# Performance work log

Hardware: AMD Instinct MI355X
Metric: run time of the kernel (lower is better)

The kernel has to match this reference:

```python
import jax, jax.numpy as jnp
import numpy as np

N, M, P, C_IN, C_OUT = 100000, 50000, 1600000, 128, 128
NEG_SLOPE = 0.2


def segment_softmax(w, seg, num):
    # numerically-stable softmax of w over segments defined by seg
    m = jax.ops.segment_max(w, seg, num_segments=num)
    e = jnp.exp(w - m[seg])
    s = jax.ops.segment_sum(e, seg, num_segments=num)
    return e / s[seg]


def setup_inputs() -> dict:
    key = jax.random.key(0)
    ks = jax.random.split(key, 8)
    scale = 1.0 / np.sqrt(C_IN)
    return {
        "X": jax.random.normal(ks[0], (N, C_IN), dtype=jnp.float32),
        "pair_v": jax.random.randint(ks[1], (P,), 0, N, dtype=jnp.int32),
        "pair_e": jax.random.randint(ks[2], (P,), 0, M, dtype=jnp.int32),
        "src_v": jax.random.randint(ks[3], (P,), 0, N, dtype=jnp.int32),
        "W_theta": jax.random.normal(ks[4], (C_OUT, C_IN), dtype=jnp.float32) * scale,
        "b_theta": jax.random.normal(ks[5], (C_OUT,), dtype=jnp.float32) * scale,
        "w_src": jax.random.normal(ks[6], (C_OUT,), dtype=jnp.float32) * scale,
        "w_dst": jax.random.normal(ks[7], (C_OUT,), dtype=jnp.float32) * scale,
    }


def reference(X, pair_v, pair_e, src_v, W_theta, b_theta, w_src, w_dst):
    # theta: linear projection (eval mode: dropout = identity, no BN)
    H = X @ W_theta.T + b_theta                      # [N, C_OUT]

    # per-pair attention scores: atten_src(H)[src] + atten_dst(H)[dst]
    s = H @ w_src                                    # [N]
    d = H @ w_dst                                    # [N]
    score = jax.nn.leaky_relu(s[src_v] + d[pair_v], NEG_SLOPE)  # [P]
    score = jnp.clip(score, 0.001, 5.0)

    # degrees
    ones = jnp.ones((P,), dtype=H.dtype)
    de = jnp.maximum(jax.ops.segment_sum(ones, pair_e, num_segments=M), 1.0)  # [M]
    dv = jnp.maximum(jax.ops.segment_sum(ones, pair_v, num_segments=N), 1.0)  # [N]

    dv_isqrt = dv ** -0.5
    Xs = H * dv_isqrt[:, None]
    Xe = jax.ops.segment_sum(Xs[pair_v], pair_e, num_segments=M) / de[:, None]  # [M, C]
    Hs = jax.ops.segment_sum(Xe[pair_e], pair_v, num_segments=N) * dv_isqrt[:, None]

    # v2v(aggr='softmax_then_sum', e2v_weight=score):
    #   v2e softmax_then_sum with unit weights == per-edge mean
    Xe1 = jax.ops.segment_sum(Hs[pair_v], pair_e, num_segments=M) / de[:, None]
    #   e2v: segment-softmax the scores per destination vertex, weighted sum
    alpha = segment_softmax(score, pair_v, N)        # [P]
    Xv1 = jax.ops.segment_sum(alpha[:, None] * Xe1[pair_e], pair_v, num_segments=N)

    # v2v(aggr='mean', v2e_aggr='softmax_then_sum'):
    #   v2e softmax_then_sum with unit weights == per-edge mean; e2v mean
    Xe2 = jax.ops.segment_sum(Xv1[pair_v], pair_e, num_segments=M) / de[:, None]
    Xv2 = jax.ops.segment_sum(Xe2[pair_e], pair_v, num_segments=N) / dv[:, None]

    # is_last=False: ELU activation (dropout identity in eval)
    return jax.nn.elu(Xv2)
```

## Files before the change

### kernel.cpp

```cpp
#include <hip/hip_runtime.h>
#include <math.h>

#define M_EDGES 50000
#define CHUNK 1024

#define NBMAX 200
#define TILE_E 4096
#define TILE_V 4096
#define CAPL_E 44
#define CAPL_V 32

typedef unsigned int u32;
typedef unsigned short u16;

__device__ __forceinline__ float bflo(u32 u) { return __uint_as_float(u << 16); }
__device__ __forceinline__ float bfhi(u32 u) { return __uint_as_float(u & 0xffff0000u); }
__device__ __forceinline__ u32 packbf(float x, float y) {
  u32 a = __float_as_uint(x); a += 0x7fffu + ((a >> 16) & 1u);
  u32 b = __float_as_uint(y); b += 0x7fffu + ((b >> 16) & 1u);
  return (a >> 16) | (b & 0xffff0000u);
}
__device__ __forceinline__ int swz(int k) { return ((k >> 2) & 7) << 2; }

__global__ __launch_bounds__(256) void bin_edge_kernel(
    const int* __restrict__ pair_e, const int* __restrict__ pair_v,
    u32* __restrict__ out, int* __restrict__ gcur,
    int P, int SE, int NB) {
  __shared__ int lcnt[NBMAX];
  __shared__ int gbase[NBMAX];
  __shared__ u32 stage[NBMAX][CAPL_E];
  const int tid = (int)threadIdx.x;
  const int p0 = blockIdx.x * TILE_E;
  const int pend = (p0 + TILE_E < P) ? p0 + TILE_E : P;
  const u32 maskE = (1u << SE) - 1u;
  for (int b = tid; b < NB; b += 256) lcnt[b] = 0;
  __syncthreads();
  for (int p = p0 + tid; p < pend; p += 256) {
    const int e = pair_e[p];
    const int v = pair_v[p];
    const int b = e >> SE;
    const u32 entry = (u32)v | (((u32)e & maskE) << 17);
    const int pos = atomicAdd(&lcnt[b], 1);
    if (pos < CAPL_E) stage[b][pos] = entry;
    else out[atomicAdd(&gcur[b], 1)] = entry;
  }
  __syncthreads();
  for (int b = tid; b < NB; b += 256) {
    const int n = lcnt[b] < CAPL_E ? lcnt[b] : CAPL_E;
    gbase[b] = atomicAdd(&gcur[b], n);
  }
  __syncthreads();
  const int wv = tid >> 6, lane = tid & 63;
  for (int b = wv; b < NB; b += 4) {
    const int n = lcnt[b] < CAPL_E ? lcnt[b] : CAPL_E;
    if (lane < n) out[gbase[b] + lane] = stage[b][lane];
  }
}

__global__ __launch_bounds__(256) void bin_vtx_kernel(
    const int* __restrict__ pair_e, const int* __restrict__ pair_v,
    const int* __restrict__ src_v,
    uint2* __restrict__ out, int* __restrict__ gcur,
    int P, int SV, int NB) {
  __shared__ int lcnt[NBMAX];
  __shared__ int gbase[NBMAX];
  __shared__ uint2 stage[NBMAX][CAPL_V];
  const int tid = (int)threadIdx.x;
  const int p0 = blockIdx.x * TILE_V;
  const int pend = (p0 + TILE_V < P) ? p0 + TILE_V : P;
  const u32 maskV = (1u << SV) - 1u;
  for (int b = tid; b < NB; b += 256) lcnt[b] = 0;
  __syncthreads();
  for (int p = p0 + tid; p < pend; p += 256) {
    const int e = pair_e[p];
    const int v = pair_v[p];
    const int s = src_v[p];
    const int b = v >> SV;
    uint2 entry;
    entry.x = ((u32)v & maskV) | ((u32)e << SV);
    entry.y = (u32)s;
    const int pos = atomicAdd(&lcnt[b], 1);
    if (pos < CAPL_V) stage[b][pos] = entry;
    else out[atomicAdd(&gcur[b], 1)] = entry;
  }
  __syncthreads();
  for (int b = tid; b < NB; b += 256) {
    const int n = lcnt[b] < CAPL_V ? lcnt[b] : CAPL_V;
    gbase[b] = atomicAdd(&gcur[b], n);
  }
  __syncthreads();
  const int wv = tid >> 6, lane = tid & 63;
  for (int b = wv; b < NB; b += 4) {
    const int n = lcnt[b] < CAPL_V ? lcnt[b] : CAPL_V;
    if (lane < n) out[gbase[b] + lane] = stage[b][lane];
  }
}

__global__ void init_gcur_kernel(int* __restrict__ ge, int* __restrict__ gv,
                                 int NBE, int NBV, int capgE, int capgV) {
  const int t = (int)threadIdx.x;
  if (t < NBE) ge[t] = t * capgE;
  if (t < NBV) gv[t] = t * capgV;
}

__global__ __launch_bounds__(256) void bucket_hist_kernel(
    const u32* __restrict__ entE, const int* __restrict__ gcurE, int* __restrict__ cnt_e,
    const uint2* __restrict__ entV, const int* __restrict__ gcurV, int* __restrict__ cnt_v,
    int NBE, int SE, int capgE, int SV, int capgV, int M, int N) {
  __shared__ int h[1024];
  const int b = (int)blockIdx.x;
  const int tid = (int)threadIdx.x;
  if (b < NBE) {
    const int nb = 1 << SE;
    for (int t = tid; t < nb; t += 256) h[t] = 0;
    __syncthreads();
    const int end = gcurE[b];
    for (int i = b * capgE + tid; i < end; i += 256)
      atomicAdd(&h[entE[i] >> 17], 1);
    __syncthreads();
    const int base = b << SE;
    for (int t = tid; t < nb; t += 256)
      if (base + t < M) cnt_e[base + t] = h[t];
  } else {
    const int bb = b - NBE;
    const int nb = 1 << SV;
    for (int t = tid; t < nb; t += 256) h[t] = 0;
    __syncthreads();
    const int end = gcurV[bb];
    const u32 mask = (1u << SV) - 1u;
    for (int i = bb * capgV + tid; i < end; i += 256)
      atomicAdd(&h[entV[i].x & mask], 1);
    __syncthreads();
    const int base = bb << SV;
    for (int t = tid; t < nb; t += 256)
      if (base + t < N) cnt_v[base + t] = h[t];
  }
}

__global__ __launch_bounds__(512) void unbin_edge_kernel(
    const u32* __restrict__ ent, const int* __restrict__ gcur,
    int* __restrict__ cur_e, int* __restrict__ edge_vtx,
    int SE, int capg) {
  const int b = blockIdx.x;
  const int end = gcur[b];
  const int ebase = b << SE;
  for (int i = b * capg + (int)threadIdx.x; i < end; i += 512) {
    const u32 w = ent[i];
    const int v = (int)(w & 0x1ffffu);
    const int e = ebase + (int)(w >> 17);
    edge_vtx[atomicAdd(&cur_e[e], 1)] = v;
  }
}

__global__ __launch_bounds__(512) void unbin_vtx_kernel(
    const uint2* __restrict__ ent, const int* __restrict__ gcur,
    int* __restrict__ cur_v, int2* __restrict__ vtx_es,
    const float* __restrict__ svec, const float* __restrict__ dvec,
    int SV, int capg) {
  const int b = blockIdx.x;
  const int end = gcur[b];
  const int vbase = b << SV;
  const u32 maskV = (1u << SV) - 1u;
  for (int i = b * capg + (int)threadIdx.x; i < end; i += 512) {
    const uint2 w = ent[i];
    const int v = vbase + (int)(w.x & maskV);
    const int e = (int)(w.x >> SV);
    float sc = svec[w.y] + dvec[v];
    sc = sc > 0.f ? sc : 0.2f * sc;
    sc = fminf(fmaxf(sc, 0.001f), 5.0f);
    vtx_es[atomicAdd(&cur_v[v], 1)] = make_int2(e, __float_as_int(__expf(sc)));
  }
}

__global__ __launch_bounds__(1024) void blocksum_kernel(
    const int* __restrict__ cnt_e, const int* __restrict__ cnt_v,
    int* __restrict__ part, int CE, int M, int N) {
  const int b = blockIdx.x;
  const int* cnt;
  int n, chunk;
  if (b < CE) { cnt = cnt_e; n = M; chunk = b; }
  else        { cnt = cnt_v; n = N; chunk = b - CE; }
  const int i = chunk * CHUNK + (int)threadIdx.x;
  int x = (i < n) ? cnt[i] : 0;
#pragma unroll
  for (int m = 32; m >= 1; m >>= 1) x += __shfl_xor(x, m, 64);
  __shared__ int ws[16];
  if ((threadIdx.x & 63) == 0) ws[threadIdx.x >> 6] = x;
  __syncthreads();
  if (threadIdx.x == 0) {
    int t = 0;
#pragma unroll
    for (int q = 0; q < 16; ++q) t += ws[q];
    part[b] = t;
  }
}

__global__ __launch_bounds__(256) void partscan_kernel(
    int* __restrict__ part, int CE, int CV,
    int* __restrict__ off_e, int* __restrict__ off_v, int M, int N) {
  __shared__ int sh[256];
  const int tid = (int)threadIdx.x;
  for (int s = 0; s < 2; ++s) {
    const int base = s ? CE : 0;
    const int count = s ? CV : CE;
    int x = (tid < count) ? part[base + tid] : 0;
    sh[tid] = x;
    __syncthreads();
    for (int ofs = 1; ofs < 256; ofs <<= 1) {
      int v = (tid >= ofs) ? sh[tid - ofs] : 0;
      __syncthreads();
      sh[tid] += v;
      __syncthreads();
    }
    if (tid < count) part[base + tid] = sh[tid] - x;
    if (tid == 0) {
      const int tot = sh[count - 1];
      if (s == 0) off_e[M] = tot; else off_v[N] = tot;
    }
    __syncthreads();
  }
}

__global__ __launch_bounds__(1024) void blockscan_kernel(
    const int* __restrict__ cnt_e, const int* __restrict__ cnt_v,
    const int* __restrict__ part,
    int* __restrict__ off_e, int* __restrict__ off_v,
    int* __restrict__ cur_e, int* __restrict__ cur_v,
    float* __restrict__ de_inv, float* __restrict__ dv_inv, float* __restrict__ dv_isqrt,
    int CE, int M, int N) {
  __shared__ int sh[CHUNK];
  const int b = blockIdx.x;
  const int tid = (int)threadIdx.x;
  const int* cnt;
  int n, chunk;
  int *off, *cur;
  float *i1, *i2;
  if (b < CE) { cnt = cnt_e; n = M; chunk = b;      off = off_e; cur = cur_e; i1 = de_inv; i2 = nullptr; }
  else        { cnt = cnt_v; n = N; chunk = b - CE; off = off_v; cur = cur_v; i1 = dv_inv; i2 = dv_isqrt; }
  const int i = chunk * CHUNK + tid;
  const int x = (i < n) ? cnt[i] : 0;
  sh[tid] = x;
  __syncthreads();
  for (int ofs = 1; ofs < CHUNK; ofs <<= 1) {
    int v = (tid >= ofs) ? sh[tid - ofs] : 0;
    __syncthreads();
    sh[tid] += v;
    __syncthreads();
  }
  if (i < n) {
    const int o = part[b] + sh[tid] - x;
    off[i] = o;
    cur[i] = o;
    const float m = (float)(x > 1 ? x : 1);
    i1[i] = 1.0f / m;
    if (i2) i2[i] = 1.0f / sqrtf(m);
  }
}

__global__ __launch_bounds__(256) void gemm_kernel(
    const float* __restrict__ X, const float* __restrict__ W,
    const float* __restrict__ bias, const float* __restrict__ wsrc,
    const float* __restrict__ wdst, const float* __restrict__ dv_isqrt,
    u16* __restrict__ Hb, float* __restrict__ s_out, float* __restrict__ d_out,
    int N) {
  __shared__ float lw[64 * 128];
  __shared__ float lx[32 * 128];
  const int tid = threadIdx.x;
  const int row0 = blockIdx.x * 32;

  for (int g = tid; g < 32 * 32; g += 256) {
    const int r = g >> 5;
    const int k4 = (g & 31) << 2;
    int rr = row0 + r;
    if (rr >= N) rr = N - 1;
    *(float4*)(lx + r * 128 + k4) = *(const float4*)(X + (size_t)rr * 128 + k4);
  }

  const int tx = tid & 31;
  const int ty = tid >> 5;
  const int c0 = tx << 2;
  const int r0 = ty << 2;
  float acc[4][4] = {};

  for (int half = 0; half < 2; ++half) {
    __syncthreads();
    for (int g = tid; g < 128 * 16; g += 256) {
      const int c = g >> 4;
      const int kk4 = (g & 15) << 2;
      const float4 v = *(const float4*)(W + (size_t)c * 128 + half * 64 + kk4);
      const int s = swz(kk4);
      lw[(kk4 + 0) * 128 + (c ^ s)] = v.x;
      lw[(kk4 + 1) * 128 + (c ^ s)] = v.y;
      lw[(kk4 + 2) * 128 + (c ^ s)] = v.z;
      lw[(kk4 + 3) * 128 + (c ^ s)] = v.w;
    }
    __syncthreads();
#pragma unroll 8
    for (int kk = 0; kk < 64; ++kk) {
      const int k = half * 64 + kk;
      const float4 wv = *(const float4*)(lw + kk * 128 + (c0 ^ swz(kk)));
      const float x0 = lx[(r0 + 0) * 128 + k];
      const float x1 = lx[(r0 + 1) * 128 + k];
      const float x2 = lx[(r0 + 2) * 128 + k];
      const float x3 = lx[(r0 + 3) * 128 + k];
      acc[0][0] += x0 * wv.x; acc[0][1] += x0 * wv.y; acc[0][2] += x0 * wv.z; acc[0][3] += x0 * wv.w;
      acc[1][0] += x1 * wv.x; acc[1][1] += x1 * wv.y; acc[1][2] += x1 * wv.z; acc[1][3] += x1 * wv.w;
      acc[2][0] += x2 * wv.x; acc[2][1] += x2 * wv.y; acc[2][2] += x2 * wv.z; acc[2][3] += x2 * wv.w;
      acc[3][0] += x3 * wv.x; acc[3][1] += x3 * wv.y; acc[3][2] += x3 * wv.z; acc[3][3] += x3 * wv.w;
    }
  }

  const float4 bv = *(const float4*)(bias + c0);
  const float4 sv = *(const float4*)(wsrc + c0);
  const float4 dv = *(const float4*)(wdst + c0);

#pragma unroll
  for (int r = 0; r < 4; ++r) {
    const int row = row0 + r0 + r;
    float4 h;
    h.x = acc[r][0] + bv.x; h.y = acc[r][1] + bv.y;
    h.z = acc[r][2] + bv.z; h.w = acc[r][3] + bv.w;
    float ps = h.x * sv.x + h.y * sv.y + h.z * sv.z + h.w * sv.w;
    float pd = h.x * dv.x + h.y * dv.y + h.z * dv.z + h.w * dv.w;
#pragma unroll
    for (int m = 16; m >= 1; m >>= 1) {
      ps += __shfl_xor(ps, m, 64);
      pd += __shfl_xor(pd, m, 64);
    }
    if (row < N) {
      const float sc = dv_isqrt[row];
      uint2 pk;
      pk.x = packbf(h.x * sc, h.y * sc);
      pk.y = packbf(h.z * sc, h.w * sc);
      *(uint2*)(Hb + (size_t)row * 128 + c0) = pk;
      if (tx == 0) { s_out[row] = ps; d_out[row] = pd; }
    }
  }
}

#define ACC8(r, p)                                         \
  a[0] += bflo((r).x) * (p); a[1] += bfhi((r).x) * (p);    \
  a[2] += bflo((r).y) * (p); a[3] += bfhi((r).y) * (p);    \
  a[4] += bflo((r).z) * (p); a[5] += bfhi((r).z) * (p);    \
  a[6] += bflo((r).w) * (p); a[7] += bfhi((r).w) * (p);

__global__ __launch_bounds__(256) void seg_pass_kernel(
    const u16* __restrict__ src, void* __restrict__ dst,
    const int* __restrict__ off, const int* __restrict__ lst, int ls,
    const float* __restrict__ post_scale,
    int nseg, int final_mode) {
  const int seg = blockIdx.x * 4 + ((int)threadIdx.x >> 6);
  if (seg >= nseg) return;
  const int lane = (int)threadIdx.x & 63;
  const int q = lane >> 4;
  const int cl = lane & 15;
  const int beg = off[seg], end = off[seg + 1];
  float a[8] = {};
  int i = beg;
  for (; i + 16 <= end; i += 16) {
    const int j0 = lst[(size_t)(i + q) * ls];
    const int j1 = lst[(size_t)(i + 4 + q) * ls];
    const int j2 = lst[(size_t)(i + 8 + q) * ls];
    const int j3 = lst[(size_t)(i + 12 + q) * ls];
    const uint4 r0 = *(const uint4*)(src + (size_t)j0 * 128 + cl * 8);
    const uint4 r1 = *(const uint4*)(src + (size_t)j1 * 128 + cl * 8);
    const uint4 r2 = *(const uint4*)(src + (size_t)j2 * 128 + cl * 8);
    const uint4 r3 = *(const uint4*)(src + (size_t)j3 * 128 + cl * 8);
    ACC8(r0, 1.0f) ACC8(r1, 1.0f) ACC8(r2, 1.0f) ACC8(r3, 1.0f)
  }
  if (i + 8 <= end) {
    const int j0 = lst[(size_t)(i + q) * ls];
    const int j1 = lst[(size_t)(i + 4 + q) * ls];
    const uint4 r0 = *(const uint4*)(src + (size_t)j0 * 128 + cl * 8);
    const uint4 r1 = *(const uint4*)(src + (size_t)j1 * 128 + cl * 8);
    ACC8(r0, 1.0f) ACC8(r1, 1.0f)
    i += 8;
  }
  if (i + 4 <= end) {
    const int j0 = lst[(size_t)(i + q) * ls];
    const uint4 r0 = *(const uint4*)(src + (size_t)j0 * 128 + cl * 8);
    ACC8(r0, 1.0f)
    i += 4;
  }
  if (i + q < end) {
    const int j0 = lst[(size_t)(i + q) * ls];
    const uint4 r0 = *(const uint4*)(src + (size_t)j0 * 128 + cl * 8);
    ACC8(r0, 1.0f)
  }
#pragma unroll
  for (int k = 0; k < 8; ++k) {
    a[k] += __shfl_xor(a[k], 16, 64);
    a[k] += __shfl_xor(a[k], 32, 64);
  }
  if (q != 0) return;
  const float ps = post_scale ? post_scale[seg] : 1.0f;
#pragma unroll
  for (int k = 0; k < 8; ++k) a[k] *= ps;
  if (final_mode) {
#pragma unroll
    for (int k = 0; k < 8; ++k) a[k] = a[k] > 0.f ? a[k] : expm1f(a[k]);
    float* o = (float*)dst + (size_t)seg * 128 + cl * 8;
    *(float4*)(o + 0) = make_float4(a[0], a[1], a[2], a[3]);
    *(float4*)(o + 4) = make_float4(a[4], a[5], a[6], a[7]);
  } else {
    uint4 pk;
    pk.x = packbf(a[0], a[1]); pk.y = packbf(a[2], a[3]);
    pk.z = packbf(a[4], a[5]); pk.w = packbf(a[6], a[7]);
    *(uint4*)((u16*)dst + (size_t)seg * 128 + cl * 8) = pk;
  }
}

__global__ __launch_bounds__(256) void attn_pass_kernel(
    const u16* __restrict__ src, u16* __restrict__ dst,
    const int* __restrict__ off, const int2* __restrict__ lst_es, int nseg) {
  const int seg = blockIdx.x * 4 + ((int)threadIdx.x >> 6);
  if (seg >= nseg) return;
  const int lane = (int)threadIdx.x & 63;
  const int q = lane >> 4;
  const int cl = lane & 15;
  const int beg = off[seg], end = off[seg + 1];
  float a[8] = {};
  float den = 0.f;
  int i = beg;
  for (; i + 16 <= end; i += 16) {
    const int2 e0 = lst_es[i + q];
    const int2 e1 = lst_es[i + 4 + q];
    const int2 e2 = lst_es[i + 8 + q];
    const int2 e3 = lst_es[i + 12 + q];
    const uint4 r0 = *(const uint4*)(src + (size_t)e0.x * 128 + cl * 8);
    const uint4 r1 = *(const uint4*)(src + (size_t)e1.x * 128 + cl * 8);
    const uint4 r2 = *(const uint4*)(src + (size_t)e2.x * 128 + cl * 8);
    const uint4 r3 = *(const uint4*)(src + (size_t)e3.x * 128 + cl * 8);
    const float s0 = __int_as_float(e0.y), s1 = __int_as_float(e1.y);
    const float s2 = __int_as_float(e2.y), s3 = __int_as_float(e3.y);
    ACC8(r0, s0) ACC8(r1, s1) ACC8(r2, s2) ACC8(r3, s3)
    den += s0 + s1 + s2 + s3;
  }
  if (i + 8 <= end) {
    const int2 e0 = lst_es[i + q];
    const int2 e1 = lst_es[i + 4 + q];
    const uint4 r0 = *(const uint4*)(src + (size_t)e0.x * 128 + cl * 8);
    const uint4 r1 = *(const uint4*)(src + (size_t)e1.x * 128 + cl * 8);
    const float s0 = __int_as_float(e0.y), s1 = __int_as_float(e1.y);
    ACC8(r0, s0) ACC8(r1, s1)
    den += s0 + s1;
    i += 8;
  }
  if (i + 4 <= end) {
    const int2 e0 = lst_es[i + q];
    const uint4 r0 = *(const uint4*)(src + (size_t)e0.x * 128 + cl * 8);
    const float s0 = __int_as_float(e0.y);
    ACC8(r0, s0)
    den += s0;
    i += 4;
  }
  if (i + q < end) {
    const int2 e0 = lst_es[i + q];
    const uint4 r0 = *(const uint4*)(src + (size_t)e0.x * 128 + cl * 8);
    const float s0 = __int_as_float(e0.y);
    ACC8(r0, s0)
    den += s0;
  }
#pragma unroll
  for (int k = 0; k < 8; ++k) {
    a[k] += __shfl_xor(a[k], 16, 64);
    a[k] += __shfl_xor(a[k], 32, 64);
  }
  den += __shfl_xor(den, 16, 64);
  den += __shfl_xor(den, 32, 64);
  const float inv = (end > beg) ? 1.0f / den : 0.0f;
  if (q != 0) return;
  uint4 pk;
  pk.x = packbf(a[0] * inv, a[1] * inv); pk.y = packbf(a[2] * inv, a[3] * inv);
  pk.z = packbf(a[4] * inv, a[5] * inv); pk.w = packbf(a[6] * inv, a[7] * inv);
  *(uint4*)(dst + (size_t)seg * 128 + cl * 8) = pk;
}

extern "C" void kernel_launch(void* const* d_in, const int* in_sizes, int n_in,
                              void* d_out, int out_size, void* d_ws, size_t ws_size,
                              hipStream_t stream) {
  const float* X      = (const float*)d_in[0];
  const int*   pair_v = (const int*)d_in[1];
  const int*   pair_e = (const int*)d_in[2];
  const int*   src_v  = (const int*)d_in[3];
  const float* W      = (const float*)d_in[4];
  const float* bias   = (const float*)d_in[5];
  const float* wsrc   = (const float*)d_in[6];
  const float* wdst   = (const float*)d_in[7];

  const int N = in_sizes[0] / 128;
  const int P = in_sizes[1];
  const int M = M_EDGES;
  const int CE = (M + CHUNK - 1) / CHUNK;
  const int CV = (N + CHUNK - 1) / CHUNK;

  int SE = 8;
  while ((((M - 1) >> SE) + 1) > NBMAX) ++SE;
  const int NBE = ((M - 1) >> SE) + 1;
  int SV = 9;
  while ((((N - 1) >> SV) + 1) > NBMAX) ++SV;
  const int NBV = ((N - 1) >> SV) + 1;
  const int capgE = P / NBE + P / (NBE * 8) + 256;
  const int capgV = P / NBV + P / (NBV * 8) + 256;

  char* w = (char*)d_ws;
  auto alloc = [&](size_t bytes) -> char* {
    char* p = w;
    w += (bytes + 255) & ~(size_t)255;
    return p;
  };
  int*   cnt_e     = (int*)alloc((size_t)M * 4);
  int*   cnt_v     = (int*)alloc((size_t)N * 4);
  int*   cur_e     = (int*)alloc((size_t)M * 4);
  int*   cur_v     = (int*)alloc((size_t)N * 4);
  int*   part      = (int*)alloc((size_t)(CE + CV) * 4);
  int*   edge_off  = (int*)alloc((size_t)(M + 1) * 4);
  int*   vtx_off   = (int*)alloc((size_t)(N + 1) * 4);
  float* de_inv    = (float*)alloc((size_t)M * 4);
  float* dv_inv    = (float*)alloc((size_t)N * 4);
  float* dv_isqrt  = (float*)alloc((size_t)N * 4);
  float* svec      = (float*)alloc((size_t)N * 4);
  float* dvec      = (float*)alloc((size_t)N * 4);
  int*   edge_vtx  = (int*)alloc((size_t)P * 4);
  int2*  vtx_es    = (int2*)alloc((size_t)P * 8);
  u16*   bufN      = (u16*)alloc((size_t)N * 128 * 2);
  u16*   bufM      = (u16*)alloc((size_t)M * 128 * 2);
  u32*   binE      = (u32*)alloc((size_t)NBE * capgE * 4);
  uint2* binV      = (uint2*)alloc((size_t)NBV * capgV * 8);
  int*   gcur_e    = (int*)alloc((size_t)NBE * 4);
  int*   gcur_v    = (int*)alloc((size_t)NBV * 4);

  init_gcur_kernel<<<1, 256, 0, stream>>>(gcur_e, gcur_v, NBE, NBV, capgE, capgV);
  bin_edge_kernel<<<(P + TILE_E - 1) / TILE_E, 256, 0, stream>>>(
      pair_e, pair_v, binE, gcur_e, P, SE, NBE);
  bin_vtx_kernel<<<(P + TILE_V - 1) / TILE_V, 256, 0, stream>>>(
      pair_e, pair_v, src_v, binV, gcur_v, P, SV, NBV);
  bucket_hist_kernel<<<NBE + NBV, 256, 0, stream>>>(
      binE, gcur_e, cnt_e, binV, gcur_v, cnt_v, NBE, SE, capgE, SV, capgV, M, N);
  blocksum_kernel<<<CE + CV, 1024, 0, stream>>>(cnt_e, cnt_v, part, CE, M, N);
  partscan_kernel<<<1, 256, 0, stream>>>(part, CE, CV, edge_off, vtx_off, M, N);
  blockscan_kernel<<<CE + CV, 1024, 0, stream>>>(cnt_e, cnt_v, part, edge_off, vtx_off,
                                                 cur_e, cur_v, de_inv, dv_inv, dv_isqrt,
                                                 CE, M, N);
  gemm_kernel<<<(N + 31) / 32, 256, 0, stream>>>(X, W, bias, wsrc, wdst, dv_isqrt,
                                                 bufN, svec, dvec, N);
  unbin_edge_kernel<<<NBE, 512, 0, stream>>>(binE, gcur_e, cur_e, edge_vtx, SE, capgE);
  unbin_vtx_kernel<<<NBV, 512, 0, stream>>>(binV, gcur_v, cur_v, vtx_es, svec, dvec,
                                            SV, capgV);

  const int gm = (M + 3) / 4;
  const int gn = (N + 3) / 4;
  seg_pass_kernel<<<gm, 256, 0, stream>>>(bufN, bufM, edge_off, edge_vtx, 1, de_inv, M, 0);
  seg_pass_kernel<<<gn, 256, 0, stream>>>(bufM, bufN, vtx_off, (const int*)vtx_es, 2, dv_isqrt, N, 0);
  seg_pass_kernel<<<gm, 256, 0, stream>>>(bufN, bufM, edge_off, edge_vtx, 1, de_inv, M, 0);
  attn_pass_kernel<<<gn, 256, 0, stream>>>(bufM, bufN, vtx_off, vtx_es, N);
  seg_pass_kernel<<<gm, 256, 0, stream>>>(bufN, bufM, edge_off, edge_vtx, 1, de_inv, M, 0);
  seg_pass_kernel<<<gn, 256, 0, stream>>>(bufM, d_out, vtx_off, (const int*)vtx_es, 2, dv_inv, N, 1);
}
```

Measured before the change: 653.4 us.

## Replace FP32 SIMT projection GEMM with split-bf16 MFMA GEMM

```diff
diff --git a/kernel.cpp b/kernel.cpp
--- a/kernel.cpp
+++ b/kernel.cpp
@@ -12,6 +12,8 @@
 
 typedef unsigned int u32;
 typedef unsigned short u16;
+typedef float f32x4 __attribute__((ext_vector_type(4)));
+typedef short bf16x8 __attribute__((ext_vector_type(8)));
 
 __device__ __forceinline__ float bflo(u32 u) { return __uint_as_float(u << 16); }
 __device__ __forceinline__ float bfhi(u32 u) { return __uint_as_float(u & 0xffff0000u); }
@@ -20,7 +22,16 @@
   u32 b = __float_as_uint(y); b += 0x7fffu + ((b >> 16) & 1u);
   return (a >> 16) | (b & 0xffff0000u);
 }
-__device__ __forceinline__ int swz(int k) { return ((k >> 2) & 7) << 2; }
+__device__ __forceinline__ u32 bf16rne(float x) {
+  u32 a = __float_as_uint(x);
+  a += 0x7fffu + ((a >> 16) & 1u);
+  return a >> 16;
+}
+__device__ __forceinline__ void bfsplit(float f, u32& h, u32& l) {
+  h = bf16rne(f);
+  const float hf = __uint_as_float(h << 16);
+  l = bf16rne(f - hf);
+}
 
 __global__ __launch_bounds__(256) void bin_edge_kernel(
     const int* __restrict__ pair_e, const int* __restrict__ pair_v,
@@ -257,84 +268,107 @@
   }
 }
 
-__global__ __launch_bounds__(256) void gemm_kernel(
-    const float* __restrict__ X, const float* __restrict__ W,
+__global__ __launch_bounds__(256) void prep_w_kernel(
+    const float* __restrict__ W, u16* __restrict__ whi, u16* __restrict__ wlo) {
+  const int i = (int)blockIdx.x * 256 + (int)threadIdx.x;
+  if (i >= 128 * 128) return;
+  u32 h, l;
+  bfsplit(W[i], h, l);
+  whi[i] = (u16)h;
+  wlo[i] = (u16)l;
+}
+
+#define XPAD 136
+__global__ __launch_bounds__(256) void gemm_mfma_kernel(
+    const float* __restrict__ X,
+    const u16* __restrict__ whi, const u16* __restrict__ wlo,
     const float* __restrict__ bias, const float* __restrict__ wsrc,
     const float* __restrict__ wdst, const float* __restrict__ dv_isqrt,
     u16* __restrict__ Hb, float* __restrict__ s_out, float* __restrict__ d_out,
     int N) {
-  __shared__ float lw[64 * 128];
-  __shared__ float lx[32 * 128];
-  const int tid = threadIdx.x;
-  const int row0 = blockIdx.x * 32;
-
-  for (int g = tid; g < 32 * 32; g += 256) {
+  __shared__ u16 xhi[64 * XPAD];
+  __shared__ u16 xlo[64 * XPAD];
+  __shared__ float sred[64];
+  __shared__ float dred[64];
+  const int tid = (int)threadIdx.x;
+  const int row0 = (int)blockIdx.x * 64;
+
+  if (tid < 64) { sred[tid] = 0.f; dred[tid] = 0.f; }
+  for (int g = tid; g < 64 * 32; g += 256) {
     const int r = g >> 5;
     const int k4 = (g & 31) << 2;
-    int rr = row0 + r;
-    if (rr >= N) rr = N - 1;
-    *(float4*)(lx + r * 128 + k4) = *(const float4*)(X + (size_t)rr * 128 + k4);
-  }
-
-  const int tx = tid & 31;
-  const int ty = tid >> 5;
-  const int c0 = tx << 2;
-  const int r0 = ty << 2;
-  float acc[4][4] = {};
-
-  for (int half = 0; half < 2; ++half) {
-    __syncthreads();
-    for (int g = tid; g < 128 * 16; g += 256) {
-      const int c = g >> 4;
-      const int kk4 = (g & 15) << 2;
-      const float4 v = *(const float4*)(W + (size_t)c * 128 + half * 64 + kk4);
-      const int s = swz(kk4);
-      lw[(kk4 + 0) * 128 + (c ^ s)] = v.x;
-      lw[(kk4 + 1) * 128 + (c ^ s)] = v.y;
-      lw[(kk4 + 2) * 128 + (c ^ s)] = v.z;
-      lw[(kk4 + 3) * 128 + (c ^ s)] = v.w;
+    int rr = row0 + r; if (rr >= N) rr = N - 1;
+    const float4 v = *(const float4*)(X + (size_t)rr * 128 + k4);
+    u32 h0, l0, h1, l1, h2, l2, h3, l3;
+    bfsplit(v.x, h0, l0); bfsplit(v.y, h1, l1);
+    bfsplit(v.z, h2, l2); bfsplit(v.w, h3, l3);
+    *(uint2*)(xhi + r * XPAD + k4) = make_uint2(h0 | (h1 << 16), h2 | (h3 << 16));
+    *(uint2*)(xlo + r * XPAD + k4) = make_uint2(l0 | (l1 << 16), l2 | (l3 << 16));
+  }
+  __syncthreads();
+
+  const int wv = tid >> 6;
+  const int l  = tid & 63;
+  const int lr = l & 15;
+  const int lg = l >> 4;
+  const int cb = wv * 32;
+
+  f32x4 zero = {0.f, 0.f, 0.f, 0.f};
+  f32x4 acc[4][2];
+#pragma unroll
+  for (int rt = 0; rt < 4; ++rt) { acc[rt][0] = zero; acc[rt][1] = zero; }
+
+#pragma unroll
+  for (int kk = 0; kk < 4; ++kk) {
+    const int kof = kk * 32 + lg * 8;
+    const bf16x8 bh0 = *(const bf16x8*)(whi + (size_t)(cb + lr) * 128 + kof);
+    const bf16x8 bh1 = *(const bf16x8*)(whi + (size_t)(cb + 16 + lr) * 128 + kof);
+    const bf16x8 bl0 = *(const bf16x8*)(wlo + (size_t)(cb + lr) * 128 + kof);
+    const bf16x8 bl1 = *(const bf16x8*)(wlo + (size_t)(cb + 16 + lr) * 128 + kof);
+#pragma unroll
+    for (int rt = 0; rt < 4; ++rt) {
+      const bf16x8 ah = *(const bf16x8*)(xhi + (rt * 16 + lr) * XPAD + kof);
+      const bf16x8 al = *(const bf16x8*)(xlo + (rt * 16 + lr) * XPAD + kof);
+      acc[rt][0] = __builtin_amdgcn_mfma_f32_16x16x32_bf16(ah, bh0, acc[rt][0], 0, 0, 0);
+      acc[rt][1] = __builtin_amdgcn_mfma_f32_16x16x32_bf16(ah, bh1, acc[rt][1], 0, 0, 0);
+      acc[rt][0] = __builtin_amdgcn_mfma_f32_16x16x32_bf16(al, bh0, acc[rt][0], 0, 0, 0);
+      acc[rt][1] = __builtin_amdgcn_mfma_f32_16x16x32_bf16(al, bh1, acc[rt][1], 0, 0, 0);
+      acc[rt][0] = __builtin_amdgcn_mfma_f32_16x16x32_bf16(ah, bl0, acc[rt][0], 0, 0, 0);
+      acc[rt][1] = __builtin_amdgcn_mfma_f32_16x16x32_bf16(ah, bl1, acc[rt][1], 0, 0, 0);
     }
-    __syncthreads();
-#pragma unroll 8
-    for (int kk = 0; kk < 64; ++kk) {
-      const int k = half * 64 + kk;
-      const float4 wv = *(const float4*)(lw + kk * 128 + (c0 ^ swz(kk)));
-      const float x0 = lx[(r0 + 0) * 128 + k];
-      const float x1 = lx[(r0 + 1) * 128 + k];
-      const float x2 = lx[(r0 + 2) * 128 + k];
-      const float x3 = lx[(r0 + 3) * 128 + k];
-      acc[0][0] += x0 * wv.x; acc[0][1] += x0 * wv.y; acc[0][2] += x0 * wv.z; acc[0][3] += x0 * wv.w;
-      acc[1][0] += x1 * wv.x; acc[1][1] += x1 * wv.y; acc[1][2] += x1 * wv.z; acc[1][3] += x1 * wv.w;
-      acc[2][0] += x2 * wv.x; acc[2][1] += x2 * wv.y; acc[2][2] += x2 * wv.z; acc[2][3] += x2 * wv.w;
-      acc[3][0] += x3 * wv.x; acc[3][1] += x3 * wv.y; acc[3][2] += x3 * wv.z; acc[3][3] += x3 * wv.w;
+  }
+
+  const int c0 = cb + lr, c1 = cb + 16 + lr;
+  const float bb0 = bias[c0], bb1 = bias[c1];
+  const float ws0 = wsrc[c0], ws1 = wsrc[c1];
+  const float wd0 = wdst[c0], wd1 = wdst[c1];
+#pragma unroll
+  for (int rt = 0; rt < 4; ++rt) {
+#pragma unroll
+    for (int j = 0; j < 4; ++j) {
+      const int rl = rt * 16 + lg * 4 + j;
+      const int row = row0 + rl;
+      const float h0 = acc[rt][0][j] + bb0;
+      const float h1 = acc[rt][1][j] + bb1;
+      float sp = h0 * ws0 + h1 * ws1;
+      float dp = h0 * wd0 + h1 * wd1;
+#pragma unroll
+      for (int m = 1; m <= 8; m <<= 1) {
+        sp += __shfl_xor(sp, m, 64);
+        dp += __shfl_xor(dp, m, 64);
+      }
+      if (lr == 0) { atomicAdd(&sred[rl], sp); atomicAdd(&dred[rl], dp); }
+      if (row < N) {
+        const float sc = dv_isqrt[row];
+        Hb[(size_t)row * 128 + c0] = (u16)bf16rne(h0 * sc);
+        Hb[(size_t)row * 128 + c1] = (u16)bf16rne(h1 * sc);
+      }
     }
   }
-
-  const float4 bv = *(const float4*)(bias + c0);
-  const float4 sv = *(const float4*)(wsrc + c0);
-  const float4 dv = *(const float4*)(wdst + c0);
-
-#pragma unroll
-  for (int r = 0; r < 4; ++r) {
-    const int row = row0 + r0 + r;
-    float4 h;
-    h.x = acc[r][0] + bv.x; h.y = acc[r][1] + bv.y;
-    h.z = acc[r][2] + bv.z; h.w = acc[r][3] + bv.w;
-    float ps = h.x * sv.x + h.y * sv.y + h.z * sv.z + h.w * sv.w;
-    float pd = h.x * dv.x + h.y * dv.y + h.z * dv.z + h.w * dv.w;
-#pragma unroll
-    for (int m = 16; m >= 1; m >>= 1) {
-      ps += __shfl_xor(ps, m, 64);
-      pd += __shfl_xor(pd, m, 64);
-    }
-    if (row < N) {
-      const float sc = dv_isqrt[row];
-      uint2 pk;
-      pk.x = packbf(h.x * sc, h.y * sc);
-      pk.y = packbf(h.z * sc, h.w * sc);
-      *(uint2*)(Hb + (size_t)row * 128 + c0) = pk;
-      if (tx == 0) { s_out[row] = ps; d_out[row] = pd; }
-    }
+  __syncthreads();
+  if (tid < 64) {
+    const int row = row0 + tid;
+    if (row < N) { s_out[row] = sred[tid]; d_out[row] = dred[tid]; }
   }
 }
 
@@ -529,7 +563,10 @@
   uint2* binV      = (uint2*)alloc((size_t)NBV * capgV * 8);
   int*   gcur_e    = (int*)alloc((size_t)NBE * 4);
   int*   gcur_v    = (int*)alloc((size_t)NBV * 4);
-
+  u16*   whi_g     = (u16*)alloc((size_t)128 * 128 * 2);
+  u16*   wlo_g     = (u16*)alloc((size_t)128 * 128 * 2);
+
+  prep_w_kernel<<<64, 256, 0, stream>>>(W, whi_g, wlo_g);
   init_gcur_kernel<<<1, 256, 0, stream>>>(gcur_e, gcur_v, NBE, NBV, capgE, capgV);
   bin_edge_kernel<<<(P + TILE_E - 1) / TILE_E, 256, 0, stream>>>(
       pair_e, pair_v, binE, gcur_e, P, SE, NBE);
@@ -542,8 +579,8 @@
   blockscan_kernel<<<CE + CV, 1024, 0, stream>>>(cnt_e, cnt_v, part, edge_off, vtx_off,
                                                  cur_e, cur_v, de_inv, dv_inv, dv_isqrt,
                                                  CE, M, N);
-  gemm_kernel<<<(N + 31) / 32, 256, 0, stream>>>(X, W, bias, wsrc, wdst, dv_isqrt,
-                                                 bufN, svec, dvec, N);
+  gemm_mfma_kernel<<<(N + 63) / 64, 256, 0, stream>>>(X, whi_g, wlo_g, bias, wsrc, wdst,
+                                                      dv_isqrt, bufN, svec, dvec, N);
   unbin_edge_kernel<<<NBE, 512, 0, stream>>>(binE, gcur_e, cur_e, edge_vtx, SE, capgE);
   unbin_vtx_kernel<<<NBV, 512, 0, stream>>>(binV, gcur_v, cur_v, vtx_es, svec, dvec,
                                             SV, capgV);
```

After: 619.8 us. 1.05x faster.
